# Optimization experiments

Measured on AMD Instinct MI355X. Metric: run time of the kernel, lower is better.

The kernel has to match this reference:

```python
import jax, jax.numpy as jnp
import numpy as np

INPUT_SIZE = 24
HIDDEN = 128
N_LAYERS = 2
OUT_SIZE = 1


def setup_inputs() -> dict:
    key = jax.random.key(0)
    ks = jax.random.split(key, 2 + 4 * N_LAYERS + 2)
    x = jax.random.normal(ks[0], (2048, 128, INPUT_SIZE), dtype=jnp.float32)
    params = {}
    s = 1.0 / np.sqrt(HIDDEN)
    idx = 1
    for l in range(N_LAYERS):
        in_dim = INPUT_SIZE if l == 0 else HIDDEN
        params[f"W_ih{l}"] = jax.random.uniform(ks[idx], (4 * HIDDEN, in_dim), minval=-s, maxval=s, dtype=jnp.float32); idx += 1
        params[f"W_hh{l}"] = jax.random.uniform(ks[idx], (4 * HIDDEN, HIDDEN), minval=-s, maxval=s, dtype=jnp.float32); idx += 1
        params[f"b_ih{l}"] = jax.random.uniform(ks[idx], (4 * HIDDEN,), minval=-s, maxval=s, dtype=jnp.float32); idx += 1
        params[f"b_hh{l}"] = jax.random.uniform(ks[idx], (4 * HIDDEN,), minval=-s, maxval=s, dtype=jnp.float32); idx += 1
    params["W_fc"] = jax.random.uniform(ks[idx], (OUT_SIZE, HIDDEN), minval=-s, maxval=s, dtype=jnp.float32); idx += 1
    params["b_fc"] = jax.random.uniform(ks[idx], (OUT_SIZE,), minval=-s, maxval=s, dtype=jnp.float32)
    return {"x": x, **params}


def _lstm_layer(x, W_ih, W_hh, b_ih, b_hh):
    # x: [B, T, in] -> outputs [B, T, H]. PyTorch gate order: i, f, g, o.
    B = x.shape[0]
    H = W_hh.shape[1]
    # precompute input projections for all timesteps: [T, B, 4H]
    xproj = jnp.einsum('bti,gi->tbg', x, W_ih) + b_ih + b_hh

    def step(carry, xp_t):
        h, c = carry
        gates = xp_t + h @ W_hh.T  # [B, 4H]
        i, f, g, o = jnp.split(gates, 4, axis=-1)
        i = jax.nn.sigmoid(i)
        f = jax.nn.sigmoid(f)
        g = jnp.tanh(g)
        o = jax.nn.sigmoid(o)
        c = f * c + i * g
        h = o * jnp.tanh(c)
        return (h, c), h

    h0 = jnp.zeros((B, H), dtype=x.dtype)
    c0 = jnp.zeros((B, H), dtype=x.dtype)
    (_, _), hs = jax.lax.scan(step, (h0, c0), xproj)
    return jnp.transpose(hs, (1, 0, 2))  # [B, T, H]


def reference(x, W_ih0, W_hh0, b_ih0, b_hh0, W_ih1, W_hh1, b_ih1, b_hh1, W_fc, b_fc):
    # Inference-mode forward: inter-layer dropout (p=0.2) is identity in eval.
    h1 = _lstm_layer(x, W_ih0, W_hh0, b_ih0, b_hh0)   # [B, T, H]
    h2 = _lstm_layer(h1, W_ih1, W_hh1, b_ih1, b_hh1)  # [B, T, H]
    last = h2[:, -1, :]                               # [B, H]
    return last @ W_fc.T + b_fc                       # [B, 1]
```

## Files before the change

### kernel.cpp

```cpp
#include <hip/hip_runtime.h>

#define TSTEPS 128
#define NIN 24
#define HD 128
#define BT 16
#define NBLK 128
#define NTH 1024

#define RS    136
#define SLOT  (BT*RS)
#define H1B   (2*SLOT)
#define W1B   (4*SLOT)
#define SM_ELTS (W1B + 65536)
#define SM_BYTES (SM_ELTS*2)

typedef _Float16 half8  __attribute__((ext_vector_type(8)));
typedef _Float16 half4v __attribute__((ext_vector_type(4)));
typedef float    floatx4 __attribute__((ext_vector_type(4)));

__device__ __forceinline__ float sigf(float x) {
    return __builtin_amdgcn_rcpf(1.0f + __expf(-x));
}
__device__ __forceinline__ float tanh_f(float x) {
    return 1.0f - 2.0f * __builtin_amdgcn_rcpf(1.0f + __expf(2.0f * x));
}

__device__ __forceinline__ half8 ldw8(const float* p) {
    const float4* q = (const float4*)p;
    float4 a = q[0], b = q[1];
    half8 r;
    r[0] = (_Float16)a.x; r[1] = (_Float16)a.y; r[2] = (_Float16)a.z; r[3] = (_Float16)a.w;
    r[4] = (_Float16)b.x; r[5] = (_Float16)b.y; r[6] = (_Float16)b.z; r[7] = (_Float16)b.w;
    return r;
}

__device__ __forceinline__ void barrier_lgkm() {
    asm volatile("s_waitcnt lgkmcnt(0)" ::: "memory");
    __builtin_amdgcn_s_barrier();
    __builtin_amdgcn_sched_barrier(0);
}

__global__ __launch_bounds__(NTH, 4)
void lstm2_fused(const float* __restrict__ x,
                 const float* __restrict__ Wih0, const float* __restrict__ Whh0,
                 const float* __restrict__ bih0, const float* __restrict__ bhh0,
                 const float* __restrict__ Wih1, const float* __restrict__ Whh1,
                 const float* __restrict__ bih1, const float* __restrict__ bhh1,
                 const float* __restrict__ Wfc,  const float* __restrict__ bfc,
                 float* __restrict__ out)
{
    extern __shared__ __align__(16) _Float16 SM[];

    const int tid = threadIdx.x;
    const int blk = blockIdx.x;
    const int wv  = tid >> 6;
    const int ln  = tid & 63;
    const int qd  = ln >> 4;
    const int nn  = ln & 15;
    const int b0  = blk * BT;

    const half8 z8 = {0, 0, 0, 0, 0, 0, 0, 0};
    const floatx4 zf4 = {0.f, 0.f, 0.f, 0.f};

    for (int i = tid * 8; i < W1B; i += NTH * 8) *(half8*)&SM[i] = z8;
    for (int i = tid; i < 512 * 32; i += NTH) {
        int g  = i >> 5;
        int k0 = (i & 31) << 2;
        float4 v = *(const float4*)(Whh1 + g * HD + k0);
        half4v h; h[0] = (_Float16)v.x; h[1] = (_Float16)v.y;
                  h[2] = (_Float16)v.z; h[3] = (_Float16)v.w;
        int dst = W1B + ((((g >> 4) & 7) * 16) + (g >> 7) * 4 + (k0 >> 5)) * 512
                      + (((k0 >> 3) & 3) * 16 + (g & 15)) * 8 + (k0 & 7);
        *(half4v*)&SM[dst] = h;
    }

    if (wv < 8) {
        const int hw_  = wv;
        const int hcol = hw_ * 16 + qd * 4;

        half8 wih0[4];
        half8 whh0[4][4];
#pragma unroll
        for (int tI = 0; tI < 4; ++tI) {
            int g = tI * HD + hw_ * 16 + nn;
            if (qd < 3) {
                wih0[tI] = ldw8(Wih0 + g * NIN + qd * 8);
            } else {
                wih0[tI] = z8;
                wih0[tI][0] = (_Float16)(bih0[g] + bhh0[g]);
            }
#pragma unroll
            for (int kk = 0; kk < 4; ++kk)
                whh0[tI][kk] = ldw8(Whh0 + g * HD + kk * 32 + qd * 8);
        }

        const float* xrow = x + (size_t)(b0 + nn) * (TSTEPS * NIN) + (qd < 3 ? qd * 8 : 0);
        float4 pf0 = *(const float4*)(xrow);
        float4 pf1 = *(const float4*)(xrow + 4);

        float cs0[4] = {0.f, 0.f, 0.f, 0.f};

        __syncthreads();

        {
            half8 ax;
            if (qd < 3) {
                ax[0] = (_Float16)pf0.x; ax[1] = (_Float16)pf0.y; ax[2] = (_Float16)pf0.z; ax[3] = (_Float16)pf0.w;
                ax[4] = (_Float16)pf1.x; ax[5] = (_Float16)pf1.y; ax[6] = (_Float16)pf1.z; ax[7] = (_Float16)pf1.w;
            } else {
                ax = z8; ax[0] = (_Float16)1.0f;
            }
            pf0 = *(const float4*)(xrow + NIN);
            pf1 = *(const float4*)(xrow + NIN + 4);

            floatx4 acc0[4];
#pragma unroll
            for (int tI = 0; tI < 4; ++tI)
                acc0[tI] = __builtin_amdgcn_mfma_f32_16x16x32_f16(wih0[tI], ax, zf4, 0, 0, 0);

            half4v hw;
#pragma unroll
            for (int r = 0; r < 4; ++r) {
                float iv = sigf(acc0[0][r]);
                float gv = tanh_f(acc0[2][r]);
                float ov = sigf(acc0[3][r]);
                float cn = iv * gv;
                cs0[r] = cn;
                hw[r] = (_Float16)(ov * tanh_f(cn));
            }
            *(half4v*)&SM[0 * SLOT + nn * RS + hcol] = hw;
        }

#pragma unroll 1
        for (int t = 1; t < TSTEPS; ++t) {
            barrier_lgkm();

            half8 ax;
            if (qd < 3) {
                ax[0] = (_Float16)pf0.x; ax[1] = (_Float16)pf0.y; ax[2] = (_Float16)pf0.z; ax[3] = (_Float16)pf0.w;
                ax[4] = (_Float16)pf1.x; ax[5] = (_Float16)pf1.y; ax[6] = (_Float16)pf1.z; ax[7] = (_Float16)pf1.w;
            } else {
                ax = z8; ax[0] = (_Float16)1.0f;
            }
            {
                const int tn = (t < TSTEPS - 1) ? t + 1 : TSTEPS - 1;
                pf0 = *(const float4*)(xrow + (size_t)tn * NIN);
                pf1 = *(const float4*)(xrow + (size_t)tn * NIN + 4);
            }

            const int h0r = ((t - 1) & 1) * SLOT;
            const int h0w = (t & 1) * SLOT;

            floatx4 acc0[4];
#pragma unroll
            for (int tI = 0; tI < 4; ++tI)
                acc0[tI] = __builtin_amdgcn_mfma_f32_16x16x32_f16(wih0[tI], ax, zf4, 0, 0, 0);

            __builtin_amdgcn_s_setprio(1);
#pragma unroll
            for (int kk = 0; kk < 4; ++kk) {
                const half8 ah = *(const half8*)&SM[h0r + nn * RS + kk * 32 + qd * 8];
#pragma unroll
                for (int tI = 0; tI < 4; ++tI)
                    acc0[tI] = __builtin_amdgcn_mfma_f32_16x16x32_f16(whh0[tI][kk], ah, acc0[tI], 0, 0, 0);
            }
            __builtin_amdgcn_s_setprio(0);

            half4v hw;
#pragma unroll
            for (int r = 0; r < 4; ++r) {
                float iv = sigf(acc0[0][r]);
                float fv = sigf(acc0[1][r]);
                float gv = tanh_f(acc0[2][r]);
                float ov = sigf(acc0[3][r]);
                float cn = fv * cs0[r] + iv * gv;
                cs0[r] = cn;
                hw[r] = (_Float16)(ov * tanh_f(cn));
            }
            *(half4v*)&SM[h0w + nn * RS + hcol] = hw;
        }

        barrier_lgkm();
        barrier_lgkm();
    } else {
        const int hw_  = wv - 8;
        const int hcol = hw_ * 16 + qd * 4;

        floatx4 bias1[4];
        half8 wih1[4][4];
#pragma unroll
        for (int tI = 0; tI < 4; ++tI) {
#pragma unroll
            for (int r = 0; r < 4; ++r)
                bias1[tI][r] = bih1[tI * HD + hcol + r] + bhh1[tI * HD + hcol + r];
            int g = tI * HD + hw_ * 16 + nn;
#pragma unroll
            for (int kk = 0; kk < 4; ++kk)
                wih1[tI][kk] = ldw8(Wih1 + g * HD + kk * 32 + qd * 8);
        }
        const int w1base = W1B + hw_ * 8192 + ln * 8;

        float cs1[4] = {0.f, 0.f, 0.f, 0.f};

        __syncthreads();

#pragma unroll 1
        for (int t = 1; t < TSTEPS; ++t) {
            barrier_lgkm();

            const int h0r = ((t - 1) & 1) * SLOT;
            const int h1r = H1B + (t & 1) * SLOT;
            const int h1w = H1B + ((t & 1) ^ 1) * SLOT;

            floatx4 acc1[4];
#pragma unroll
            for (int tI = 0; tI < 4; ++tI) acc1[tI] = bias1[tI];

            __builtin_amdgcn_s_setprio(1);
#pragma unroll
            for (int kk = 0; kk < 4; ++kk) {
                const half8 ah = *(const half8*)&SM[h0r + nn * RS + kk * 32 + qd * 8];
#pragma unroll
                for (int tI = 0; tI < 4; ++tI)
                    acc1[tI] = __builtin_amdgcn_mfma_f32_16x16x32_f16(wih1[tI][kk], ah, acc1[tI], 0, 0, 0);
            }
#pragma unroll
            for (int kk = 0; kk < 4; ++kk) {
                const half8 a2 = *(const half8*)&SM[h1r + nn * RS + kk * 32 + qd * 8];
#pragma unroll
                for (int tI = 0; tI < 4; ++tI) {
                    const half8 w1 = *(const half8*)&SM[w1base + (tI * 4 + kk) * 512];
                    acc1[tI] = __builtin_amdgcn_mfma_f32_16x16x32_f16(w1, a2, acc1[tI], 0, 0, 0);
                }
            }
            __builtin_amdgcn_s_setprio(0);

            half4v hw;
#pragma unroll
            for (int r = 0; r < 4; ++r) {
                float iv = sigf(acc1[0][r]);
                float fv = sigf(acc1[1][r]);
                float gv = tanh_f(acc1[2][r]);
                float ov = sigf(acc1[3][r]);
                float cn = fv * cs1[r] + iv * gv;
                cs1[r] = cn;
                hw[r] = (_Float16)(ov * tanh_f(cn));
            }
            *(half4v*)&SM[h1w + nn * RS + hcol] = hw;
        }

        barrier_lgkm();
        {
            floatx4 acc1[4];
#pragma unroll
            for (int tI = 0; tI < 4; ++tI) acc1[tI] = bias1[tI];
#pragma unroll
            for (int kk = 0; kk < 4; ++kk) {
                const half8 ah = *(const half8*)&SM[SLOT + nn * RS + kk * 32 + qd * 8];
#pragma unroll
                for (int tI = 0; tI < 4; ++tI)
                    acc1[tI] = __builtin_amdgcn_mfma_f32_16x16x32_f16(wih1[tI][kk], ah, acc1[tI], 0, 0, 0);
            }
#pragma unroll
            for (int kk = 0; kk < 4; ++kk) {
                const half8 a2 = *(const half8*)&SM[H1B + nn * RS + kk * 32 + qd * 8];
#pragma unroll
                for (int tI = 0; tI < 4; ++tI) {
                    const half8 w1 = *(const half8*)&SM[w1base + (tI * 4 + kk) * 512];
                    acc1[tI] = __builtin_amdgcn_mfma_f32_16x16x32_f16(w1, a2, acc1[tI], 0, 0, 0);
                }
            }
            half4v hw;
#pragma unroll
            for (int r = 0; r < 4; ++r) {
                float iv = sigf(acc1[0][r]);
                float fv = sigf(acc1[1][r]);
                float gv = tanh_f(acc1[2][r]);
                float ov = sigf(acc1[3][r]);
                float cn = fv * cs1[r] + iv * gv;
                hw[r] = (_Float16)(ov * tanh_f(cn));
            }
            *(half4v*)&SM[H1B + SLOT + nn * RS + hcol] = hw;
        }
        barrier_lgkm();
    }

    if (tid < 512) {
        int b = tid >> 5, sub = tid & 31;
        const _Float16* hp = &SM[H1B + SLOT + b * RS + sub * 4];
        const float4 wv4 = *(const float4*)(Wfc + sub * 4);
        float s = (float)hp[0] * wv4.x + (float)hp[1] * wv4.y
                + (float)hp[2] * wv4.z + (float)hp[3] * wv4.w;
        s += __shfl_down(s, 16, 32);
        s += __shfl_down(s, 8, 32);
        s += __shfl_down(s, 4, 32);
        s += __shfl_down(s, 2, 32);
        s += __shfl_down(s, 1, 32);
        if (sub == 0) out[b0 + b] = s + bfc[0];
    }
}

extern "C" void kernel_launch(void* const* d_in, const int* in_sizes, int n_in,
                              void* d_out, int out_size, void* d_ws, size_t ws_size,
                              hipStream_t stream) {
    static bool attr_set = false;
    if (!attr_set) {
        hipFuncSetAttribute(reinterpret_cast<const void*>(&lstm2_fused),
                            hipFuncAttributeMaxDynamicSharedMemorySize, SM_BYTES);
        attr_set = true;
    }
    const float* x    = (const float*)d_in[0];
    const float* Wih0 = (const float*)d_in[1];
    const float* Whh0 = (const float*)d_in[2];
    const float* bih0 = (const float*)d_in[3];
    const float* bhh0 = (const float*)d_in[4];
    const float* Wih1 = (const float*)d_in[5];
    const float* Whh1 = (const float*)d_in[6];
    const float* bih1 = (const float*)d_in[7];
    const float* bhh1 = (const float*)d_in[8];
    const float* Wfc  = (const float*)d_in[9];
    const float* bfc  = (const float*)d_in[10];
    float* out = (float*)d_out;

    lstm2_fused<<<dim3(NBLK), dim3(NTH), SM_BYTES, stream>>>(
        x, Wih0, Whh0, bih0, bhh0, Wih1, Whh1, bih1, bhh1, Wfc, bfc, out);
}
```

Before: 319.6 us.

## Pipeline layer-1 input projection one step ahead using triple-buffered layer-0 states

Restructures the wavefront-specialized two-layer recurrence so layer 1 computes its input projection (W_ih1·h0) for the next step right after finishing its recurrent part, off the critical path. Layer-0 hidden states move to a three-slot ring buffer so layer 0 can run one step further ahead. The aim is to shorten the per-step critical path of the slower layer-1 wavefronts, which previously did 32 MFMAs per step against 20 for layer 0. The cost is one extra LDS slot, a 130-iteration loop with branches, and two extra barrier steps.

```diff
diff --git a/kernel.cpp b/kernel.cpp
--- a/kernel.cpp
+++ b/kernel.cpp
@@ -9,8 +9,8 @@
 
 #define RS    136
 #define SLOT  (BT*RS)
-#define H1B   (2*SLOT)
-#define W1B   (4*SLOT)
+#define H1B   (3*SLOT)
+#define W1B   (5*SLOT)
 #define SM_ELTS (W1B + 65536)
 #define SM_BYTES (SM_ELTS*2)
 
@@ -99,89 +99,60 @@
         float4 pf1 = *(const float4*)(xrow + 4);
 
         float cs0[4] = {0.f, 0.f, 0.f, 0.f};
+        int wr3 = 0, p3 = 2;
 
         __syncthreads();
 
-        {
-            half8 ax;
-            if (qd < 3) {
-                ax[0] = (_Float16)pf0.x; ax[1] = (_Float16)pf0.y; ax[2] = (_Float16)pf0.z; ax[3] = (_Float16)pf0.w;
-                ax[4] = (_Float16)pf1.x; ax[5] = (_Float16)pf1.y; ax[6] = (_Float16)pf1.z; ax[7] = (_Float16)pf1.w;
-            } else {
-                ax = z8; ax[0] = (_Float16)1.0f;
-            }
-            pf0 = *(const float4*)(xrow + NIN);
-            pf1 = *(const float4*)(xrow + NIN + 4);
-
-            floatx4 acc0[4];
-#pragma unroll
-            for (int tI = 0; tI < 4; ++tI)
-                acc0[tI] = __builtin_amdgcn_mfma_f32_16x16x32_f16(wih0[tI], ax, zf4, 0, 0, 0);
-
-            half4v hw;
-#pragma unroll
-            for (int r = 0; r < 4; ++r) {
-                float iv = sigf(acc0[0][r]);
-                float gv = tanh_f(acc0[2][r]);
-                float ov = sigf(acc0[3][r]);
-                float cn = iv * gv;
-                cs0[r] = cn;
-                hw[r] = (_Float16)(ov * tanh_f(cn));
-            }
-            *(half4v*)&SM[0 * SLOT + nn * RS + hcol] = hw;
-        }
-
 #pragma unroll 1
-        for (int t = 1; t < TSTEPS; ++t) {
+        for (int t = 0; t < 130; ++t) {
+            if (t < TSTEPS) {
+                half8 ax;
+                if (qd < 3) {
+                    ax[0] = (_Float16)pf0.x; ax[1] = (_Float16)pf0.y; ax[2] = (_Float16)pf0.z; ax[3] = (_Float16)pf0.w;
+                    ax[4] = (_Float16)pf1.x; ax[5] = (_Float16)pf1.y; ax[6] = (_Float16)pf1.z; ax[7] = (_Float16)pf1.w;
+                } else {
+                    ax = z8; ax[0] = (_Float16)1.0f;
+                }
+                {
+                    const int tn = (t < TSTEPS - 1) ? t + 1 : TSTEPS - 1;
+                    pf0 = *(const float4*)(xrow + (size_t)tn * NIN);
+                    pf1 = *(const float4*)(xrow + (size_t)tn * NIN + 4);
+                }
+
+                floatx4 acc0[4];
+#pragma unroll
+                for (int tI = 0; tI < 4; ++tI)
+                    acc0[tI] = __builtin_amdgcn_mfma_f32_16x16x32_f16(wih0[tI], ax, zf4, 0, 0, 0);
+
+                if (t > 0) {
+                    __builtin_amdgcn_s_setprio(1);
+#pragma unroll
+                    for (int kk = 0; kk < 4; ++kk) {
+                        const half8 ah = *(const half8*)&SM[p3 * SLOT + nn * RS + kk * 32 + qd * 8];
+#pragma unroll
+                        for (int tI = 0; tI < 4; ++tI)
+                            acc0[tI] = __builtin_amdgcn_mfma_f32_16x16x32_f16(whh0[tI][kk], ah, acc0[tI], 0, 0, 0);
+                    }
+                    __builtin_amdgcn_s_setprio(0);
+                }
+
+                half4v hw;
+#pragma unroll
+                for (int r = 0; r < 4; ++r) {
+                    float iv = sigf(acc0[0][r]);
+                    float fv = sigf(acc0[1][r]);
+                    float gv = tanh_f(acc0[2][r]);
+                    float ov = sigf(acc0[3][r]);
+                    float cn = (t > 0 ? fv * cs0[r] : 0.f) + iv * gv;
+                    cs0[r] = cn;
+                    hw[r] = (_Float16)(ov * tanh_f(cn));
+                }
+                *(half4v*)&SM[wr3 * SLOT + nn * RS + hcol] = hw;
+            }
+            p3 = wr3;
+            wr3 = (wr3 == 2) ? 0 : wr3 + 1;
             barrier_lgkm();
-
-            half8 ax;
-            if (qd < 3) {
-                ax[0] = (_Float16)pf0.x; ax[1] = (_Float16)pf0.y; ax[2] = (_Float16)pf0.z; ax[3] = (_Float16)pf0.w;
-                ax[4] = (_Float16)pf1.x; ax[5] = (_Float16)pf1.y; ax[6] = (_Float16)pf1.z; ax[7] = (_Float16)pf1.w;
-            } else {
-                ax = z8; ax[0] = (_Float16)1.0f;
-            }
-            {
-                const int tn = (t < TSTEPS - 1) ? t + 1 : TSTEPS - 1;
-                pf0 = *(const float4*)(xrow + (size_t)tn * NIN);
-                pf1 = *(const float4*)(xrow + (size_t)tn * NIN + 4);
-            }
-
-            const int h0r = ((t - 1) & 1) * SLOT;
-            const int h0w = (t & 1) * SLOT;
-
-            floatx4 acc0[4];
-#pragma unroll
-            for (int tI = 0; tI < 4; ++tI)
-                acc0[tI] = __builtin_amdgcn_mfma_f32_16x16x32_f16(wih0[tI], ax, zf4, 0, 0, 0);
-
-            __builtin_amdgcn_s_setprio(1);
-#pragma unroll
-            for (int kk = 0; kk < 4; ++kk) {
-                const half8 ah = *(const half8*)&SM[h0r + nn * RS + kk * 32 + qd * 8];
-#pragma unroll
-                for (int tI = 0; tI < 4; ++tI)
-                    acc0[tI] = __builtin_amdgcn_mfma_f32_16x16x32_f16(whh0[tI][kk], ah, acc0[tI], 0, 0, 0);
-            }
-            __builtin_amdgcn_s_setprio(0);
-
-            half4v hw;
-#pragma unroll
-            for (int r = 0; r < 4; ++r) {
-                float iv = sigf(acc0[0][r]);
-                float fv = sigf(acc0[1][r]);
-                float gv = tanh_f(acc0[2][r]);
-                float ov = sigf(acc0[3][r]);
-                float cn = fv * cs0[r] + iv * gv;
-                cs0[r] = cn;
-                hw[r] = (_Float16)(ov * tanh_f(cn));
-            }
-            *(half4v*)&SM[h0w + nn * RS + hcol] = hw;
-        }
-
-        barrier_lgkm();
-        barrier_lgkm();
+        }
     } else {
         const int hw_  = wv - 8;
         const int hcol = hw_ * 16 + qd * 4;
@@ -201,88 +172,57 @@
         const int w1base = W1B + hw_ * 8192 + ln * 8;
 
         float cs1[4] = {0.f, 0.f, 0.f, 0.f};
+        floatx4 pAcc[4];
+        int wr3 = 0, p3 = 2;
 
         __syncthreads();
 
 #pragma unroll 1
-        for (int t = 1; t < TSTEPS; ++t) {
+        for (int t = 0; t < 130; ++t) {
+            if (t >= 2) {
+                const int h1r = H1B + ((t + 1) & 1) * SLOT;
+                const int h1w = H1B + (t & 1) * SLOT;
+
+                __builtin_amdgcn_s_setprio(1);
+#pragma unroll
+                for (int kk = 0; kk < 4; ++kk) {
+                    const half8 a2 = *(const half8*)&SM[h1r + nn * RS + kk * 32 + qd * 8];
+#pragma unroll
+                    for (int tI = 0; tI < 4; ++tI) {
+                        const half8 w1 = *(const half8*)&SM[w1base + (tI * 4 + kk) * 512];
+                        pAcc[tI] = __builtin_amdgcn_mfma_f32_16x16x32_f16(w1, a2, pAcc[tI], 0, 0, 0);
+                    }
+                }
+                __builtin_amdgcn_s_setprio(0);
+
+                half4v hw;
+#pragma unroll
+                for (int r = 0; r < 4; ++r) {
+                    float iv = sigf(pAcc[0][r]);
+                    float fv = sigf(pAcc[1][r]);
+                    float gv = tanh_f(pAcc[2][r]);
+                    float ov = sigf(pAcc[3][r]);
+                    float cn = fv * cs1[r] + iv * gv;
+                    cs1[r] = cn;
+                    hw[r] = (_Float16)(ov * tanh_f(cn));
+                }
+                *(half4v*)&SM[h1w + nn * RS + hcol] = hw;
+            }
+
+            if (t >= 1 && t <= 128) {
+#pragma unroll
+                for (int kk = 0; kk < 4; ++kk) {
+                    const half8 ah = *(const half8*)&SM[p3 * SLOT + nn * RS + kk * 32 + qd * 8];
+#pragma unroll
+                    for (int tI = 0; tI < 4; ++tI)
+                        pAcc[tI] = __builtin_amdgcn_mfma_f32_16x16x32_f16(
+                            wih1[tI][kk], ah, (kk == 0 ? bias1[tI] : pAcc[tI]), 0, 0, 0);
+                }
+            }
+            p3 = wr3;
+            wr3 = (wr3 == 2) ? 0 : wr3 + 1;
             barrier_lgkm();
-
-            const int h0r = ((t - 1) & 1) * SLOT;
-            const int h1r = H1B + (t & 1) * SLOT;
-            const int h1w = H1B + ((t & 1) ^ 1) * SLOT;
-
-            floatx4 acc1[4];
-#pragma unroll
-            for (int tI = 0; tI < 4; ++tI) acc1[tI] = bias1[tI];
-
-            __builtin_amdgcn_s_setprio(1);
-#pragma unroll
-            for (int kk = 0; kk < 4; ++kk) {
-                const half8 ah = *(const half8*)&SM[h0r + nn * RS + kk * 32 + qd * 8];
-#pragma unroll
-                for (int tI = 0; tI < 4; ++tI)
-                    acc1[tI] = __builtin_amdgcn_mfma_f32_16x16x32_f16(wih1[tI][kk], ah, acc1[tI], 0, 0, 0);
-            }
-#pragma unroll
-            for (int kk = 0; kk < 4; ++kk) {
-                const half8 a2 = *(const half8*)&SM[h1r + nn * RS + kk * 32 + qd * 8];
-#pragma unroll
-                for (int tI = 0; tI < 4; ++tI) {
-                    const half8 w1 = *(const half8*)&SM[w1base + (tI * 4 + kk) * 512];
-                    acc1[tI] = __builtin_amdgcn_mfma_f32_16x16x32_f16(w1, a2, acc1[tI], 0, 0, 0);
-                }
-            }
-            __builtin_amdgcn_s_setprio(0);
-
-            half4v hw;
-#pragma unroll
-            for (int r = 0; r < 4; ++r) {
-                float iv = sigf(acc1[0][r]);
-                float fv = sigf(acc1[1][r]);
-                float gv = tanh_f(acc1[2][r]);
-                float ov = sigf(acc1[3][r]);
-                float cn = fv * cs1[r] + iv * gv;
-                cs1[r] = cn;
-                hw[r] = (_Float16)(ov * tanh_f(cn));
-            }
-            *(half4v*)&SM[h1w + nn * RS + hcol] = hw;
-        }
-
-        barrier_lgkm();
-        {
-            floatx4 acc1[4];
-#pragma unroll
-            for (int tI = 0; tI < 4; ++tI) acc1[tI] = bias1[tI];
-#pragma unroll
-            for (int kk = 0; kk < 4; ++kk) {
-                const half8 ah = *(const half8*)&SM[SLOT + nn * RS + kk * 32 + qd * 8];
-#pragma unroll
-                for (int tI = 0; tI < 4; ++tI)
-                    acc1[tI] = __builtin_amdgcn_mfma_f32_16x16x32_f16(wih1[tI][kk], ah, acc1[tI], 0, 0, 0);
-            }
-#pragma unroll
-            for (int kk = 0; kk < 4; ++kk) {
-                const half8 a2 = *(const half8*)&SM[H1B + nn * RS + kk * 32 + qd * 8];
-#pragma unroll
-                for (int tI = 0; tI < 4; ++tI) {
-                    const half8 w1 = *(const half8*)&SM[w1base + (tI * 4 + kk) * 512];
-                    acc1[tI] = __builtin_amdgcn_mfma_f32_16x16x32_f16(w1, a2, acc1[tI], 0, 0, 0);
-                }
-            }
-            half4v hw;
-#pragma unroll
-            for (int r = 0; r < 4; ++r) {
-                float iv = sigf(acc1[0][r]);
-                float fv = sigf(acc1[1][r]);
-                float gv = tanh_f(acc1[2][r]);
-                float ov = sigf(acc1[3][r]);
-                float cn = fv * cs1[r] + iv * gv;
-                hw[r] = (_Float16)(ov * tanh_f(cn));
-            }
-            *(half4v*)&SM[H1B + SLOT + nn * RS + hcol] = hw;
-        }
-        barrier_lgkm();
+        }
     }
 
     if (tid < 512) {
```

Measured after the change: 337.3 us. +5.5%, slower.

## Stream pre-converted fp16 W_hh1 from global memory with register double-buffering

Applied to the files above, without the earlier changes.

Adds a small pre-kernel that converts W_hh1 to fp16 in the MFMA-friendly swizzled layout and writes it to the workspace. The layer-1 waves then load those weights straight from global/L2 into two register buffers, prefetching the next k-slices during the MFMAs, instead of keeping them in LDS. The separate final timestep is folded into the main loop. The intent is to remove the per-block W_hh1 staging into LDS and the LDS read traffic on the recurrent path, at the cost of exposing global-load latency inside the serial time loop and an extra kernel launch.

```diff
diff --git a/kernel.cpp b/kernel.cpp
--- a/kernel.cpp
+++ b/kernel.cpp
@@ -10,9 +10,13 @@
 #define RS    136
 #define SLOT  (BT*RS)
 #define H1B   (2*SLOT)
-#define W1B   (4*SLOT)
-#define SM_ELTS (W1B + 65536)
-#define SM_BYTES (SM_ELTS*2)
+#define HPAN  (4*SLOT)
+#define DYN_WG 86016
+#define W1B   HPAN
+#define SM_ELTS_LDS (W1B + 65536)
+#define DYN_LDSPAN (SM_ELTS_LDS*2)
+
+#define WS_NEED (512*128*2)
 
 typedef _Float16 half8  __attribute__((ext_vector_type(8)));
 typedef _Float16 half4v __attribute__((ext_vector_type(4)));
@@ -40,6 +44,22 @@
     __builtin_amdgcn_sched_barrier(0);
 }
 
+__global__ __launch_bounds__(256)
+void wcvt(const float* __restrict__ Whh1, _Float16* __restrict__ wsw)
+{
+    int i = blockIdx.x * 256 + threadIdx.x;
+    if (i >= 512 * 32) return;
+    int g  = i >> 5;
+    int k0 = (i & 31) << 2;
+    float4 v = *(const float4*)(Whh1 + g * HD + k0);
+    half4v h; h[0] = (_Float16)v.x; h[1] = (_Float16)v.y;
+              h[2] = (_Float16)v.z; h[3] = (_Float16)v.w;
+    int dst = ((((g >> 4) & 7) * 16) + (g >> 7) * 4 + (k0 >> 5)) * 512
+            + (((k0 >> 3) & 3) * 16 + (g & 15)) * 8 + (k0 & 7);
+    *(half4v*)&wsw[dst] = h;
+}
+
+template<int WG>
 __global__ __launch_bounds__(NTH, 4)
 void lstm2_fused(const float* __restrict__ x,
                  const float* __restrict__ Wih0, const float* __restrict__ Whh0,
@@ -47,7 +67,7 @@
                  const float* __restrict__ Wih1, const float* __restrict__ Whh1,
                  const float* __restrict__ bih1, const float* __restrict__ bhh1,
                  const float* __restrict__ Wfc,  const float* __restrict__ bfc,
-                 float* __restrict__ out)
+                 float* __restrict__ out, const _Float16* __restrict__ wsw)
 {
     extern __shared__ __align__(16) _Float16 SM[];
 
@@ -62,16 +82,18 @@
     const half8 z8 = {0, 0, 0, 0, 0, 0, 0, 0};
     const floatx4 zf4 = {0.f, 0.f, 0.f, 0.f};
 
-    for (int i = tid * 8; i < W1B; i += NTH * 8) *(half8*)&SM[i] = z8;
-    for (int i = tid; i < 512 * 32; i += NTH) {
-        int g  = i >> 5;
-        int k0 = (i & 31) << 2;
-        float4 v = *(const float4*)(Whh1 + g * HD + k0);
-        half4v h; h[0] = (_Float16)v.x; h[1] = (_Float16)v.y;
-                  h[2] = (_Float16)v.z; h[3] = (_Float16)v.w;
-        int dst = W1B + ((((g >> 4) & 7) * 16) + (g >> 7) * 4 + (k0 >> 5)) * 512
-                      + (((k0 >> 3) & 3) * 16 + (g & 15)) * 8 + (k0 & 7);
-        *(half4v*)&SM[dst] = h;
+    for (int i = tid * 8; i < HPAN; i += NTH * 8) *(half8*)&SM[i] = z8;
+    if constexpr (WG == 0) {
+        for (int i = tid; i < 512 * 32; i += NTH) {
+            int g  = i >> 5;
+            int k0 = (i & 31) << 2;
+            float4 v = *(const float4*)(Whh1 + g * HD + k0);
+            half4v h; h[0] = (_Float16)v.x; h[1] = (_Float16)v.y;
+                      h[2] = (_Float16)v.z; h[3] = (_Float16)v.w;
+            int dst = W1B + ((((g >> 4) & 7) * 16) + (g >> 7) * 4 + (k0 >> 5)) * 512
+                          + (((k0 >> 3) & 3) * 16 + (g & 15)) * 8 + (k0 & 7);
+            *(half4v*)&SM[dst] = h;
+        }
     }
 
     if (wv < 8) {
@@ -198,14 +220,25 @@
             for (int kk = 0; kk < 4; ++kk)
                 wih1[tI][kk] = ldw8(Wih1 + g * HD + kk * 32 + qd * 8);
         }
+
+        const _Float16* w1g = (WG == 1) ? (wsw + hw_ * 8192 + ln * 8) : nullptr;
         const int w1base = W1B + hw_ * 8192 + ln * 8;
 
+        half8 wS0[4], wS1[4];
+        auto ldw1 = [&](half8* buf, int kk) {
+#pragma unroll
+            for (int tI = 0; tI < 4; ++tI)
+                buf[tI] = *(const half8*)(w1g + (tI * 4 + kk) * 512);
+        };
+
         float cs1[4] = {0.f, 0.f, 0.f, 0.f};
 
         __syncthreads();
 
+        if constexpr (WG == 1) { ldw1(wS0, 0); ldw1(wS1, 1); }
+
 #pragma unroll 1
-        for (int t = 1; t < TSTEPS; ++t) {
+        for (int t = 1; t <= TSTEPS; ++t) {
             barrier_lgkm();
 
             const int h0r = ((t - 1) & 1) * SLOT;
@@ -227,10 +260,19 @@
 #pragma unroll
             for (int kk = 0; kk < 4; ++kk) {
                 const half8 a2 = *(const half8*)&SM[h1r + nn * RS + kk * 32 + qd * 8];
-#pragma unroll
-                for (int tI = 0; tI < 4; ++tI) {
-                    const half8 w1 = *(const half8*)&SM[w1base + (tI * 4 + kk) * 512];
-                    acc1[tI] = __builtin_amdgcn_mfma_f32_16x16x32_f16(w1, a2, acc1[tI], 0, 0, 0);
+                if constexpr (WG == 1) {
+                    const half8* wb = (kk & 1) ? wS1 : wS0;
+#pragma unroll
+                    for (int tI = 0; tI < 4; ++tI)
+                        acc1[tI] = __builtin_amdgcn_mfma_f32_16x16x32_f16(wb[tI], a2, acc1[tI], 0, 0, 0);
+                    if (kk == 0) ldw1(wS0, 2);
+                    if (kk == 1) ldw1(wS1, 3);
+                } else {
+#pragma unroll
+                    for (int tI = 0; tI < 4; ++tI) {
+                        const half8 w1 = *(const half8*)&SM[w1base + (tI * 4 + kk) * 512];
+                        acc1[tI] = __builtin_amdgcn_mfma_f32_16x16x32_f16(w1, a2, acc1[tI], 0, 0, 0);
+                    }
                 }
             }
             __builtin_amdgcn_s_setprio(0);
@@ -247,41 +289,12 @@
                 hw[r] = (_Float16)(ov * tanh_f(cn));
             }
             *(half4v*)&SM[h1w + nn * RS + hcol] = hw;
-        }
-
-        barrier_lgkm();
-        {
-            floatx4 acc1[4];
-#pragma unroll
-            for (int tI = 0; tI < 4; ++tI) acc1[tI] = bias1[tI];
-#pragma unroll
-            for (int kk = 0; kk < 4; ++kk) {
-                const half8 ah = *(const half8*)&SM[SLOT + nn * RS + kk * 32 + qd * 8];
-#pragma unroll
-                for (int tI = 0; tI < 4; ++tI)
-                    acc1[tI] = __builtin_amdgcn_mfma_f32_16x16x32_f16(wih1[tI][kk], ah, acc1[tI], 0, 0, 0);
-            }
-#pragma unroll
-            for (int kk = 0; kk < 4; ++kk) {
-                const half8 a2 = *(const half8*)&SM[H1B + nn * RS + kk * 32 + qd * 8];
-#pragma unroll
-                for (int tI = 0; tI < 4; ++tI) {
-                    const half8 w1 = *(const half8*)&SM[w1base + (tI * 4 + kk) * 512];
-                    acc1[tI] = __builtin_amdgcn_mfma_f32_16x16x32_f16(w1, a2, acc1[tI], 0, 0, 0);
-                }
-            }
-            half4v hw;
-#pragma unroll
-            for (int r = 0; r < 4; ++r) {
-                float iv = sigf(acc1[0][r]);
-                float fv = sigf(acc1[1][r]);
-                float gv = tanh_f(acc1[2][r]);
-                float ov = sigf(acc1[3][r]);
-                float cn = fv * cs1[r] + iv * gv;
-                hw[r] = (_Float16)(ov * tanh_f(cn));
-            }
-            *(half4v*)&SM[H1B + SLOT + nn * RS + hcol] = hw;
-        }
+
+            if constexpr (WG == 1) {
+                if (t < TSTEPS) { ldw1(wS0, 0); ldw1(wS1, 1); }
+            }
+        }
+
         barrier_lgkm();
     }
 
@@ -305,8 +318,10 @@
                               hipStream_t stream) {
     static bool attr_set = false;
     if (!attr_set) {
-        hipFuncSetAttribute(reinterpret_cast<const void*>(&lstm2_fused),
-                            hipFuncAttributeMaxDynamicSharedMemorySize, SM_BYTES);
+        hipFuncSetAttribute(reinterpret_cast<const void*>(&lstm2_fused<1>),
+                            hipFuncAttributeMaxDynamicSharedMemorySize, DYN_WG);
+        hipFuncSetAttribute(reinterpret_cast<const void*>(&lstm2_fused<0>),
+                            hipFuncAttributeMaxDynamicSharedMemorySize, DYN_LDSPAN);
         attr_set = true;
     }
     const float* x    = (const float*)d_in[0];
@@ -322,6 +337,13 @@
     const float* bfc  = (const float*)d_in[10];
     float* out = (float*)d_out;
 
-    lstm2_fused<<<dim3(NBLK), dim3(NTH), SM_BYTES, stream>>>(
-        x, Wih0, Whh0, bih0, bhh0, Wih1, Whh1, bih1, bhh1, Wfc, bfc, out);
-}
+    if (ws_size >= WS_NEED) {
+        _Float16* wsw = (_Float16*)d_ws;
+        wcvt<<<dim3(64), dim3(256), 0, stream>>>(Whh1, wsw);
+        lstm2_fused<1><<<dim3(NBLK), dim3(NTH), DYN_WG, stream>>>(
+            x, Wih0, Whh0, bih0, bhh0, Wih1, Whh1, bih1, bhh1, Wfc, bfc, out, wsw);
+    } else {
+        lstm2_fused<0><<<dim3(NBLK), dim3(NTH), DYN_LDSPAN, stream>>>(
+            x, Wih0, Whh0, bih0, bhh0, Wih1, Whh1, bih1, bhh1, Wfc, bfc, out, nullptr);
+    }
+}
```

After: 737.9 us. 2.31x slower.
